# Kernel tuning notes

Measured on AMD Instinct MI355X. Metric: run time of the kernel, lower is better.

Reference implementation:

```python
import jax, jax.numpy as jnp
import numpy as np

B, D, L, H = 512, 512, 32, 300  # batch, input_dim, latent_dim, hidden_dim


def setup_inputs() -> dict:
    key = jax.random.key(0)
    ks = jax.random.split(key, 16)
    s = lambda k, *sh: jax.random.normal(k, sh, dtype=jnp.float32) * 0.05
    return {
        "x": jax.random.normal(ks[0], (B, D), dtype=jnp.float32),
        "eps": jax.random.normal(ks[1], (B, L), dtype=jnp.float32),
        "W": jax.random.normal(ks[2], (D, L), dtype=jnp.float32),  # mask (get_generator_mask -> W)
        "qz_w1": s(ks[3], D, H), "qz_b1": s(ks[4], H),
        "qz_w2": s(ks[5], H, H), "qz_b2": s(ks[6], H),
        "zm_w": s(ks[7], H, L), "zm_b": s(ks[8], L),
        "zl_w": s(ks[9], H, L), "zl_b": s(ks[10], L),
        "gen_w1": s(ks[11], L, H),               # no bias (bias=False)
        "gen_w2": s(ks[12], H, H), "gen_b2": s(ks[13], H),
        "col_w": s(ks[14], D, H), "col_b": s(ks[15], D),  # stacked column_means Linears
    }


def reference(x, eps, W, qz_w1, qz_b1, qz_w2, qz_b2, zm_w, zm_b, zl_w, zl_b,
              gen_w1, gen_w2, gen_b2, col_w, col_b):
    # encode
    h = jax.nn.relu(x @ qz_w1 + qz_b1)
    h = jax.nn.relu(h @ qz_w2 + qz_b2)
    z_mean = h @ zm_w + zm_b
    z_log_var = h @ zl_w + zl_b
    # reparameterize (eps supplied as input)
    z = z_mean + eps * jnp.exp(0.5 * z_log_var)
    # decode: per-column masked generator MLP, batched over columns j
    masked = W[:, None, :] * z[None, :, :]                 # [D, B, L]
    g = jax.nn.relu(jnp.einsum('jbl,lh->jbh', masked, gen_w1))
    g = jax.nn.relu(jnp.einsum('jbh,hk->jbk', g, gen_w2) + gen_b2)
    x_rec = jnp.einsum('jbh,jh->jb', g, col_w) + col_b[:, None]  # [D, B]
    x_mean = x_rec.T                                       # [B, D]
    return (x_mean, z, z_mean, z_log_var)
```

## Files before the change

kernel.cpp:

```cpp
#include <hip/hip_runtime.h>

#define B_ 512
#define D_ 512
#define L_ 32
#define H_ 300
#define NT 19
#define NS 10
#define G1S 308

typedef unsigned short ushort_t;
typedef __bf16 bf16x8 __attribute__((ext_vector_type(8)));
typedef float f32x4 __attribute__((ext_vector_type(4)));

union B8 { ushort_t u[8]; uint4 q; bf16x8 v; uint2 d[2]; __bf16 b[8]; };

__device__ __forceinline__ void split8(const float* fv, B8& hi, B8& lo) {
    #pragma unroll
    for (int i = 0; i < 8; ++i) {
        __bf16 h = (__bf16)fv[i];
        hi.b[i] = h;
        lo.b[i] = (__bf16)(fv[i] - (float)h);
    }
}

__global__ __launch_bounds__(64) void prep_kernel(
        const float* __restrict__ gw1, const float* __restrict__ gw2,
        const float* __restrict__ qw1, const float* __restrict__ qw2,
        const float* __restrict__ zmw, const float* __restrict__ zlw,
        ushort_t* __restrict__ gw1f, ushort_t* __restrict__ gw2f,
        ushort_t* __restrict__ w1hi, ushort_t* __restrict__ w1lo,
        ushort_t* __restrict__ w2hi, ushort_t* __restrict__ w2lo,
        ushort_t* __restrict__ w3hi, ushort_t* __restrict__ w3lo) {
    int blk = blockIdx.x;
    int l = threadIdx.x, grp = l >> 4, li = l & 15;
    if (blk < 209) {
        const float* src; int K, nt, s; ushort_t* dst;
        if (blk < 19) { nt = blk; s = 0; src = gw1; K = 32; dst = gw1f + (nt * 64 + l) * 8; }
        else { int i = blk - 19; nt = i / 10; s = i % 10; src = gw2; K = 300;
               dst = gw2f + ((nt * 10 + s) * 64 + l) * 8; }
        int n = nt * 16 + li;
        B8 V;
        #pragma unroll
        for (int i = 0; i < 8; ++i) {
            int k = 32 * s + 8 * grp + i;
            V.b[i] = (__bf16)((k < K && n < H_) ? src[k * H_ + n] : 0.f);
        }
        *reinterpret_cast<uint4*>(dst) = V.q;
    } else {
        const float* src = nullptr; int K, N, nt, s, stacked = 0;
        ushort_t *dh, *dl;
        if (blk < 513)      { int i = blk - 209; nt = i / 16; s = i % 16; src = qw1; K = 512; N = 300;
                              dh = w1hi + ((nt * 16 + s) * 64 + l) * 8; dl = w1lo + ((nt * 16 + s) * 64 + l) * 8; }
        else if (blk < 703) { int i = blk - 513; nt = i / 10; s = i % 10; src = qw2; K = 300; N = 300;
                              dh = w2hi + ((nt * 10 + s) * 64 + l) * 8; dl = w2lo + ((nt * 10 + s) * 64 + l) * 8; }
        else                { int i = blk - 703; nt = i / 10; s = i % 10; K = 300; N = 64; stacked = 1;
                              dh = w3hi + ((nt * 10 + s) * 64 + l) * 8; dl = w3lo + ((nt * 10 + s) * 64 + l) * 8; }
        int n = nt * 16 + li;
        float fv[8];
        #pragma unroll
        for (int i = 0; i < 8; ++i) {
            int k = 32 * s + 8 * grp + i;
            float v = 0.f;
            if (k < K && n < N) {
                if (!stacked) v = src[k * N + n];
                else          v = (n < 32) ? zmw[k * 32 + n] : zlw[k * 32 + (n - 32)];
            }
            fv[i] = v;
        }
        B8 Vh, Vl;
        split8(fv, Vh, Vl);
        *reinterpret_cast<uint4*>(dh) = Vh.q;
        *reinterpret_cast<uint4*>(dl) = Vl.q;
    }
}

template<int KSTEPS, bool RELU>
__global__ __launch_bounds__(256) void enc_gemm_f32(const float* __restrict__ A, int lda,
        const ushort_t* __restrict__ Whi, const ushort_t* __restrict__ Wlo,
        const float* __restrict__ bias, float* __restrict__ out, int ldo,
        int Ncols, int ntiles) {
    const int tid = threadIdx.x;
    const int w = tid >> 6, lane = tid & 63;
    const int grp = lane >> 4, li = lane & 15;
    const int r0 = blockIdx.x * 16;
    const int nt = blockIdx.y * 4 + w;
    const bool active = nt < ntiles;

    f32x4 acc = {0.f, 0.f, 0.f, 0.f};
    for (int s = 0; s < KSTEPS; ++s) {
        int kb = 32 * s + 8 * grp;
        B8 Ah, Al;
        if (kb + 8 <= lda) {
            const float* ap = A + (size_t)(r0 + li) * lda + kb;
            float4 f0 = *reinterpret_cast<const float4*>(ap);
            float4 f1 = *reinterpret_cast<const float4*>(ap + 4);
            float fv[8] = {f0.x, f0.y, f0.z, f0.w, f1.x, f1.y, f1.z, f1.w};
            split8(fv, Ah, Al);
        } else {
            Ah.q = make_uint4(0, 0, 0, 0);
            Al.q = make_uint4(0, 0, 0, 0);
        }
        if (active) {
            bf16x8 bh = *reinterpret_cast<const bf16x8*>(
                Whi + ((size_t)(nt * KSTEPS + s) * 64 + lane) * 8);
            bf16x8 bl = *reinterpret_cast<const bf16x8*>(
                Wlo + ((size_t)(nt * KSTEPS + s) * 64 + lane) * 8);
            acc = __builtin_amdgcn_mfma_f32_16x16x32_bf16(Ah.v, bh, acc, 0, 0, 0);
            acc = __builtin_amdgcn_mfma_f32_16x16x32_bf16(Al.v, bh, acc, 0, 0, 0);
            acc = __builtin_amdgcn_mfma_f32_16x16x32_bf16(Ah.v, bl, acc, 0, 0, 0);
        }
    }
    if (active) {
        int h = nt * 16 + li;
        float bv = (bias != nullptr && h < Ncols) ? bias[h] : 0.f;
        #pragma unroll
        for (int r = 0; r < 4; ++r) {
            float v = acc[r] + bv;
            if (RELU) v = fmaxf(v, 0.f);
            if (h >= Ncols) v = 0.f;
            out[(size_t)(r0 + 4 * grp + r) * ldo + h] = v;
        }
    }
}

__global__ __launch_bounds__(256) void enc3_reparam(const float* __restrict__ h2,
        const ushort_t* __restrict__ w3hi, const ushort_t* __restrict__ w3lo,
        const float* __restrict__ zmb, const float* __restrict__ zlb,
        const float* __restrict__ eps, float* __restrict__ out, float* __restrict__ zb) {
    __shared__ float zs[16][64];
    const int tid = threadIdx.x;
    const int w = tid >> 6, lane = tid & 63;
    const int grp = lane >> 4, li = lane & 15;
    const int r0 = blockIdx.x * 16;

    f32x4 acc = {0.f, 0.f, 0.f, 0.f};
    for (int s = 0; s < 10; ++s) {
        int kb = 32 * s + 8 * grp;
        B8 Ah, Al;
        if (kb + 8 <= 304) {
            const float* ap = h2 + (size_t)(r0 + li) * 304 + kb;
            float4 f0 = *reinterpret_cast<const float4*>(ap);
            float4 f1 = *reinterpret_cast<const float4*>(ap + 4);
            float fv[8] = {f0.x, f0.y, f0.z, f0.w, f1.x, f1.y, f1.z, f1.w};
            split8(fv, Ah, Al);
        } else {
            Ah.q = make_uint4(0, 0, 0, 0);
            Al.q = make_uint4(0, 0, 0, 0);
        }
        bf16x8 bh = *reinterpret_cast<const bf16x8*>(w3hi + ((size_t)(w * 10 + s) * 64 + lane) * 8);
        bf16x8 bl = *reinterpret_cast<const bf16x8*>(w3lo + ((size_t)(w * 10 + s) * 64 + lane) * 8);
        acc = __builtin_amdgcn_mfma_f32_16x16x32_bf16(Ah.v, bh, acc, 0, 0, 0);
        acc = __builtin_amdgcn_mfma_f32_16x16x32_bf16(Al.v, bh, acc, 0, 0, 0);
        acc = __builtin_amdgcn_mfma_f32_16x16x32_bf16(Ah.v, bl, acc, 0, 0, 0);
    }
    #pragma unroll
    for (int r = 0; r < 4; ++r) zs[4 * grp + r][w * 16 + li] = acc[r];
    __syncthreads();

    for (int idx = tid; idx < 512; idx += 256) {
        int m = idx >> 5, l2 = idx & 31;
        int row = r0 + m;
        float zm = zs[m][l2] + zmb[l2];
        float zl = zs[m][32 + l2] + zlb[l2];
        float zv = zm + eps[row * 32 + l2] * expf(0.5f * zl);
        out[B_ * D_ + row * 32 + l2] = zv;
        out[B_ * D_ + B_ * L_ + row * 32 + l2] = zm;
        out[B_ * D_ + 2 * B_ * L_ + row * 32 + l2] = zl;
        zb[row * 32 + l2] = zv;
    }
}

__global__ __launch_bounds__(256, 3) void decode_kernel(
        const float* __restrict__ z, const float* __restrict__ Wmask,
        const ushort_t* __restrict__ gw1f, const ushort_t* __restrict__ gw2f,
        const float* __restrict__ gb2, const float* __restrict__ colw,
        const float* __restrict__ colb, float* __restrict__ xmean) {
    __shared__ __align__(16) ushort_t g1s[64 * G1S + 16];
    __shared__ float xpart[4][64];

    const int j    = blockIdx.y;
    const int b0   = blockIdx.x * 64;
    const int tid  = threadIdx.x;
    const int w    = tid >> 6;
    const int lane = tid & 63;
    const int grp  = lane >> 4, li = lane & 15;
    const int nlocal = (w == 3) ? 4 : 5;

    B8 bm[4];
    {
        const float* wp = Wmask + (size_t)j * L_ + 8 * grp;
        float4 w0 = *reinterpret_cast<const float4*>(wp);
        float4 w1 = *reinterpret_cast<const float4*>(wp + 4);
        float wv[8] = {w0.x, w0.y, w0.z, w0.w, w1.x, w1.y, w1.z, w1.w};
        #pragma unroll
        for (int mt = 0; mt < 4; ++mt) {
            const float* zp = z + (size_t)(b0 + mt * 16 + li) * L_ + 8 * grp;
            float4 z0 = *reinterpret_cast<const float4*>(zp);
            float4 z1 = *reinterpret_cast<const float4*>(zp + 4);
            float zv[8] = {z0.x, z0.y, z0.z, z0.w, z1.x, z1.y, z1.z, z1.w};
            #pragma unroll
            for (int i = 0; i < 8; ++i) bm[mt].b[i] = (__bf16)(wv[i] * zv[i]);
        }
        for (int idx = tid; idx < 272; idx += 256) {
            if (idx < 256) g1s[(idx >> 2) * G1S + 304 + (idx & 3)] = 0;
            else           g1s[64 * G1S + (idx - 256)] = 0;
        }
    }
    __syncthreads();

    #pragma unroll
    for (int ntl = 0; ntl < 5; ++ntl) {
        if (ntl < nlocal) {
            int nt = w * 5 + ntl;
            bf16x8 ga = *reinterpret_cast<const bf16x8*>(gw1f + (nt * 64 + lane) * 8);
            #pragma unroll
            for (int mt = 0; mt < 4; ++mt) {
                f32x4 c = {0.f, 0.f, 0.f, 0.f};
                c = __builtin_amdgcn_mfma_f32_16x16x32_bf16(ga, bm[mt].v, c, 0, 0, 0);
                B8 P;
                #pragma unroll
                for (int r = 0; r < 4; ++r) P.b[r] = (__bf16)fmaxf(c[r], 0.f);
                *reinterpret_cast<uint2*>(&g1s[(mt * 16 + li) * G1S + nt * 16 + 4 * grp]) = P.d[0];
            }
        }
    }
    __syncthreads();

    {
        f32x4 acc[4][5];
        #pragma unroll
        for (int mt = 0; mt < 4; ++mt)
            #pragma unroll
            for (int n = 0; n < 5; ++n) acc[mt][n] = {0.f, 0.f, 0.f, 0.f};

        const size_t lane8 = (size_t)lane * 8;
        for (int s = 0; s < NS; ++s) {
            B8 af[4];
            #pragma unroll
            for (int mt = 0; mt < 4; ++mt) {
                const ushort_t* p = &g1s[(mt * 16 + li) * G1S + 32 * s + 8 * grp];
                af[mt].d[0] = *reinterpret_cast<const uint2*>(p);
                af[mt].d[1] = *reinterpret_cast<const uint2*>(p + 4);
            }
            #pragma unroll
            for (int ntl = 0; ntl < 5; ++ntl) {
                if (ntl < nlocal) {
                    bf16x8 bfr = *reinterpret_cast<const bf16x8*>(
                        gw2f + (size_t)((w * 5 + ntl) * NS + s) * 512 + lane8);
                    #pragma unroll
                    for (int mt = 0; mt < 4; ++mt)
                        acc[mt][ntl] = __builtin_amdgcn_mfma_f32_16x16x32_bf16(
                            af[mt].v, bfr, acc[mt][ntl], 0, 0, 0);
                }
            }
        }

        float partial[4][4] = {};
        #pragma unroll
        for (int ntl = 0; ntl < 5; ++ntl) {
            if (ntl < nlocal) {
                int h = (w * 5 + ntl) * 16 + li;
                float bias = 0.f, fac = 0.f;
                if (h < H_) { bias = gb2[h]; fac = colw[j * H_ + h]; }
                #pragma unroll
                for (int mt = 0; mt < 4; ++mt)
                    #pragma unroll
                    for (int r = 0; r < 4; ++r)
                        partial[mt][r] += fmaxf(acc[mt][ntl][r] + bias, 0.f) * fac;
            }
        }
        #pragma unroll
        for (int mt = 0; mt < 4; ++mt)
            #pragma unroll
            for (int r = 0; r < 4; ++r) {
                float v = partial[mt][r];
                v += __shfl_xor(v, 1);
                v += __shfl_xor(v, 2);
                v += __shfl_xor(v, 4);
                v += __shfl_xor(v, 8);
                if (li == 0) xpart[w][mt * 16 + 4 * grp + r] = v;
            }
    }
    __syncthreads();

    if (tid < 64) {
        float v = colb[j];
        #pragma unroll
        for (int ww = 0; ww < 4; ++ww) v += xpart[ww][tid];
        xmean[(size_t)(b0 + tid) * D_ + j] = v;
    }
}

extern "C" void kernel_launch(void* const* d_in, const int* in_sizes, int n_in,
                              void* d_out, int out_size, void* d_ws, size_t ws_size,
                              hipStream_t stream) {
    const float* x     = (const float*)d_in[0];
    const float* eps   = (const float*)d_in[1];
    const float* Wm    = (const float*)d_in[2];
    const float* qz_w1 = (const float*)d_in[3];
    const float* qz_b1 = (const float*)d_in[4];
    const float* qz_w2 = (const float*)d_in[5];
    const float* qz_b2 = (const float*)d_in[6];
    const float* zm_w  = (const float*)d_in[7];
    const float* zm_b  = (const float*)d_in[8];
    const float* zl_w  = (const float*)d_in[9];
    const float* zl_b  = (const float*)d_in[10];
    const float* gw1   = (const float*)d_in[11];
    const float* gw2   = (const float*)d_in[12];
    const float* gb2   = (const float*)d_in[13];
    const float* colw  = (const float*)d_in[14];
    const float* colb  = (const float*)d_in[15];
    float* out = (float*)d_out;
    char* ws = (char*)d_ws;

    ushort_t* gw1f = (ushort_t*)(ws + 0);
    ushort_t* gw2f = (ushort_t*)(ws + 19456);
    ushort_t* w1hi = (ushort_t*)(ws + 214016);
    ushort_t* w1lo = (ushort_t*)(ws + 525312);
    ushort_t* w2hi = (ushort_t*)(ws + 836608);
    ushort_t* w2lo = (ushort_t*)(ws + 1031168);
    ushort_t* w3hi = (ushort_t*)(ws + 1225728);
    ushort_t* w3lo = (ushort_t*)(ws + 1266688);
    float*    h1   = (float*)(ws + 1307648);
    float*    h2   = (float*)(ws + 214016);
    float*    zb   = (float*)(ws + 1930240);

    prep_kernel<<<743, 64, 0, stream>>>(gw1, gw2, qz_w1, qz_w2, zm_w, zl_w,
                                        gw1f, gw2f, w1hi, w1lo, w2hi, w2lo, w3hi, w3lo);
    enc_gemm_f32<16, true><<<dim3(32, 5), 256, 0, stream>>>(
        x, 512, w1hi, w1lo, qz_b1, h1, 304, 300, NT);
    enc_gemm_f32<10, true><<<dim3(32, 5), 256, 0, stream>>>(
        h1, 304, w2hi, w2lo, qz_b2, h2, 304, 300, NT);
    enc3_reparam<<<32, 256, 0, stream>>>(h2, w3hi, w3lo, zm_b, zl_b, eps, out, zb);
    decode_kernel<<<dim3(8, 512), 256, 0, stream>>>(zb, Wm, gw1f, gw2f, gb2, colw, colb, out);
}
```

Before: 111.9 us.

## Fuse three encoder GEMMs and reparameterization into one kernel with LDS intermediates

```diff
diff --git a/kernel.cpp b/kernel.cpp
--- a/kernel.cpp
+++ b/kernel.cpp
@@ -7,6 +7,7 @@
 #define NT 19
 #define NS 10
 #define G1S 308
+#define HS 312
 
 typedef unsigned short ushort_t;
 typedef __bf16 bf16x8 __attribute__((ext_vector_type(8)));
@@ -74,94 +75,146 @@
     }
 }
 
-template<int KSTEPS, bool RELU>
-__global__ __launch_bounds__(256) void enc_gemm_f32(const float* __restrict__ A, int lda,
-        const ushort_t* __restrict__ Whi, const ushort_t* __restrict__ Wlo,
-        const float* __restrict__ bias, float* __restrict__ out, int ldo,
-        int Ncols, int ntiles) {
+__global__ __launch_bounds__(256) void fused_encoder(
+        const float* __restrict__ x,
+        const ushort_t* __restrict__ w1hi, const ushort_t* __restrict__ w1lo,
+        const ushort_t* __restrict__ w2hi, const ushort_t* __restrict__ w2lo,
+        const ushort_t* __restrict__ w3hi, const ushort_t* __restrict__ w3lo,
+        const float* __restrict__ b1, const float* __restrict__ b2,
+        const float* __restrict__ zmb, const float* __restrict__ zlb,
+        const float* __restrict__ eps, float* __restrict__ out,
+        float* __restrict__ zb) {
+    __shared__ __align__(16) ushort_t hs1_hi[16 * HS + 16], hs1_lo[16 * HS + 16];
+    __shared__ __align__(16) ushort_t hs2_hi[16 * HS + 16], hs2_lo[16 * HS + 16];
+    __shared__ float zs2[64][17];
+
     const int tid = threadIdx.x;
     const int w = tid >> 6, lane = tid & 63;
     const int grp = lane >> 4, li = lane & 15;
     const int r0 = blockIdx.x * 16;
-    const int nt = blockIdx.y * 4 + w;
-    const bool active = nt < ntiles;
-
-    f32x4 acc = {0.f, 0.f, 0.f, 0.f};
-    for (int s = 0; s < KSTEPS; ++s) {
-        int kb = 32 * s + 8 * grp;
-        B8 Ah, Al;
-        if (kb + 8 <= lda) {
-            const float* ap = A + (size_t)(r0 + li) * lda + kb;
+    const int nlocal = (w == 3) ? 4 : 5;
+
+    for (int idx = tid; idx < 16 * 8 + 16; idx += 256) {
+        int off = (idx < 128) ? ((idx >> 3) * HS + 304 + (idx & 7)) : (16 * HS + (idx - 128));
+        hs1_hi[off] = 0; hs1_lo[off] = 0; hs2_hi[off] = 0; hs2_lo[off] = 0;
+    }
+    __syncthreads();
+
+    {
+        f32x4 acc[5];
+        #pragma unroll
+        for (int i = 0; i < 5; ++i) acc[i] = {0.f, 0.f, 0.f, 0.f};
+        for (int s = 0; s < 16; ++s) {
+            const float* ap = x + (size_t)(r0 + li) * 512 + 32 * s + 8 * grp;
             float4 f0 = *reinterpret_cast<const float4*>(ap);
             float4 f1 = *reinterpret_cast<const float4*>(ap + 4);
             float fv[8] = {f0.x, f0.y, f0.z, f0.w, f1.x, f1.y, f1.z, f1.w};
-            split8(fv, Ah, Al);
-        } else {
-            Ah.q = make_uint4(0, 0, 0, 0);
-            Al.q = make_uint4(0, 0, 0, 0);
-        }
-        if (active) {
-            bf16x8 bh = *reinterpret_cast<const bf16x8*>(
-                Whi + ((size_t)(nt * KSTEPS + s) * 64 + lane) * 8);
-            bf16x8 bl = *reinterpret_cast<const bf16x8*>(
-                Wlo + ((size_t)(nt * KSTEPS + s) * 64 + lane) * 8);
-            acc = __builtin_amdgcn_mfma_f32_16x16x32_bf16(Ah.v, bh, acc, 0, 0, 0);
-            acc = __builtin_amdgcn_mfma_f32_16x16x32_bf16(Al.v, bh, acc, 0, 0, 0);
-            acc = __builtin_amdgcn_mfma_f32_16x16x32_bf16(Ah.v, bl, acc, 0, 0, 0);
-        }
-    }
-    if (active) {
-        int h = nt * 16 + li;
-        float bv = (bias != nullptr && h < Ncols) ? bias[h] : 0.f;
-        #pragma unroll
-        for (int r = 0; r < 4; ++r) {
-            float v = acc[r] + bv;
-            if (RELU) v = fmaxf(v, 0.f);
-            if (h >= Ncols) v = 0.f;
-            out[(size_t)(r0 + 4 * grp + r) * ldo + h] = v;
-        }
-    }
-}
-
-__global__ __launch_bounds__(256) void enc3_reparam(const float* __restrict__ h2,
-        const ushort_t* __restrict__ w3hi, const ushort_t* __restrict__ w3lo,
-        const float* __restrict__ zmb, const float* __restrict__ zlb,
-        const float* __restrict__ eps, float* __restrict__ out, float* __restrict__ zb) {
-    __shared__ float zs[16][64];
-    const int tid = threadIdx.x;
-    const int w = tid >> 6, lane = tid & 63;
-    const int grp = lane >> 4, li = lane & 15;
-    const int r0 = blockIdx.x * 16;
-
-    f32x4 acc = {0.f, 0.f, 0.f, 0.f};
-    for (int s = 0; s < 10; ++s) {
-        int kb = 32 * s + 8 * grp;
-        B8 Ah, Al;
-        if (kb + 8 <= 304) {
-            const float* ap = h2 + (size_t)(r0 + li) * 304 + kb;
-            float4 f0 = *reinterpret_cast<const float4*>(ap);
-            float4 f1 = *reinterpret_cast<const float4*>(ap + 4);
-            float fv[8] = {f0.x, f0.y, f0.z, f0.w, f1.x, f1.y, f1.z, f1.w};
-            split8(fv, Ah, Al);
-        } else {
-            Ah.q = make_uint4(0, 0, 0, 0);
-            Al.q = make_uint4(0, 0, 0, 0);
-        }
-        bf16x8 bh = *reinterpret_cast<const bf16x8*>(w3hi + ((size_t)(w * 10 + s) * 64 + lane) * 8);
-        bf16x8 bl = *reinterpret_cast<const bf16x8*>(w3lo + ((size_t)(w * 10 + s) * 64 + lane) * 8);
-        acc = __builtin_amdgcn_mfma_f32_16x16x32_bf16(Ah.v, bh, acc, 0, 0, 0);
-        acc = __builtin_amdgcn_mfma_f32_16x16x32_bf16(Al.v, bh, acc, 0, 0, 0);
-        acc = __builtin_amdgcn_mfma_f32_16x16x32_bf16(Ah.v, bl, acc, 0, 0, 0);
-    }
-    #pragma unroll
-    for (int r = 0; r < 4; ++r) zs[4 * grp + r][w * 16 + li] = acc[r];
+            B8 Bh, Bl;
+            split8(fv, Bh, Bl);
+            #pragma unroll
+            for (int ntl = 0; ntl < 5; ++ntl) {
+                if (ntl < nlocal) {
+                    int nt = w * 5 + ntl;
+                    bf16x8 Ah = *reinterpret_cast<const bf16x8*>(
+                        w1hi + ((size_t)(nt * 16 + s) * 64 + lane) * 8);
+                    bf16x8 Al = *reinterpret_cast<const bf16x8*>(
+                        w1lo + ((size_t)(nt * 16 + s) * 64 + lane) * 8);
+                    acc[ntl] = __builtin_amdgcn_mfma_f32_16x16x32_bf16(Ah, Bh.v, acc[ntl], 0, 0, 0);
+                    acc[ntl] = __builtin_amdgcn_mfma_f32_16x16x32_bf16(Al, Bh.v, acc[ntl], 0, 0, 0);
+                    acc[ntl] = __builtin_amdgcn_mfma_f32_16x16x32_bf16(Ah, Bl.v, acc[ntl], 0, 0, 0);
+                }
+            }
+        }
+        #pragma unroll
+        for (int ntl = 0; ntl < 5; ++ntl) {
+            if (ntl < nlocal) {
+                int nt = w * 5 + ntl;
+                B8 Ph, Pl;
+                #pragma unroll
+                for (int r = 0; r < 4; ++r) {
+                    int h = nt * 16 + 4 * grp + r;
+                    float v = (h < H_) ? fmaxf(acc[ntl][r] + b1[h], 0.f) : 0.f;
+                    __bf16 hb = (__bf16)v;
+                    Ph.b[r] = hb;
+                    Pl.b[r] = (__bf16)(v - (float)hb);
+                }
+                int off = li * HS + nt * 16 + 4 * grp;
+                *reinterpret_cast<uint2*>(&hs1_hi[off]) = Ph.d[0];
+                *reinterpret_cast<uint2*>(&hs1_lo[off]) = Pl.d[0];
+            }
+        }
+    }
+    __syncthreads();
+
+    {
+        f32x4 acc[5];
+        #pragma unroll
+        for (int i = 0; i < 5; ++i) acc[i] = {0.f, 0.f, 0.f, 0.f};
+        for (int s = 0; s < NS; ++s) {
+            int off = li * HS + 32 * s + 8 * grp;
+            B8 Bh, Bl;
+            Bh.q = *reinterpret_cast<const uint4*>(&hs1_hi[off]);
+            Bl.q = *reinterpret_cast<const uint4*>(&hs1_lo[off]);
+            #pragma unroll
+            for (int ntl = 0; ntl < 5; ++ntl) {
+                if (ntl < nlocal) {
+                    int nt = w * 5 + ntl;
+                    bf16x8 Ah = *reinterpret_cast<const bf16x8*>(
+                        w2hi + ((size_t)(nt * 10 + s) * 64 + lane) * 8);
+                    bf16x8 Al = *reinterpret_cast<const bf16x8*>(
+                        w2lo + ((size_t)(nt * 10 + s) * 64 + lane) * 8);
+                    acc[ntl] = __builtin_amdgcn_mfma_f32_16x16x32_bf16(Ah, Bh.v, acc[ntl], 0, 0, 0);
+                    acc[ntl] = __builtin_amdgcn_mfma_f32_16x16x32_bf16(Al, Bh.v, acc[ntl], 0, 0, 0);
+                    acc[ntl] = __builtin_amdgcn_mfma_f32_16x16x32_bf16(Ah, Bl.v, acc[ntl], 0, 0, 0);
+                }
+            }
+        }
+        #pragma unroll
+        for (int ntl = 0; ntl < 5; ++ntl) {
+            if (ntl < nlocal) {
+                int nt = w * 5 + ntl;
+                B8 Ph, Pl;
+                #pragma unroll
+                for (int r = 0; r < 4; ++r) {
+                    int h = nt * 16 + 4 * grp + r;
+                    float v = (h < H_) ? fmaxf(acc[ntl][r] + b2[h], 0.f) : 0.f;
+                    __bf16 hb = (__bf16)v;
+                    Ph.b[r] = hb;
+                    Pl.b[r] = (__bf16)(v - (float)hb);
+                }
+                int off = li * HS + nt * 16 + 4 * grp;
+                *reinterpret_cast<uint2*>(&hs2_hi[off]) = Ph.d[0];
+                *reinterpret_cast<uint2*>(&hs2_lo[off]) = Pl.d[0];
+            }
+        }
+    }
+    __syncthreads();
+
+    {
+        f32x4 acc = {0.f, 0.f, 0.f, 0.f};
+        for (int s = 0; s < NS; ++s) {
+            int off = li * HS + 32 * s + 8 * grp;
+            B8 Bh, Bl;
+            Bh.q = *reinterpret_cast<const uint4*>(&hs2_hi[off]);
+            Bl.q = *reinterpret_cast<const uint4*>(&hs2_lo[off]);
+            bf16x8 Ah = *reinterpret_cast<const bf16x8*>(
+                w3hi + ((size_t)(w * 10 + s) * 64 + lane) * 8);
+            bf16x8 Al = *reinterpret_cast<const bf16x8*>(
+                w3lo + ((size_t)(w * 10 + s) * 64 + lane) * 8);
+            acc = __builtin_amdgcn_mfma_f32_16x16x32_bf16(Ah, Bh.v, acc, 0, 0, 0);
+            acc = __builtin_amdgcn_mfma_f32_16x16x32_bf16(Al, Bh.v, acc, 0, 0, 0);
+            acc = __builtin_amdgcn_mfma_f32_16x16x32_bf16(Ah, Bl.v, acc, 0, 0, 0);
+        }
+        #pragma unroll
+        for (int r = 0; r < 4; ++r) zs2[w * 16 + 4 * grp + r][li] = acc[r];
+    }
     __syncthreads();
 
     for (int idx = tid; idx < 512; idx += 256) {
         int m = idx >> 5, l2 = idx & 31;
         int row = r0 + m;
-        float zm = zs[m][l2] + zmb[l2];
-        float zl = zs[m][32 + l2] + zlb[l2];
+        float zm = zs2[l2][m] + zmb[l2];
+        float zl = zs2[32 + l2][m] + zlb[l2];
         float zv = zm + eps[row * 32 + l2] * expf(0.5f * zl);
         out[B_ * D_ + row * 32 + l2] = zv;
         out[B_ * D_ + B_ * L_ + row * 32 + l2] = zm;
@@ -208,24 +261,28 @@
     }
     __syncthreads();
 
-    #pragma unroll
-    for (int ntl = 0; ntl < 5; ++ntl) {
-        if (ntl < nlocal) {
-            int nt = w * 5 + ntl;
-            bf16x8 ga = *reinterpret_cast<const bf16x8*>(gw1f + (nt * 64 + lane) * 8);
-            #pragma unroll
-            for (int mt = 0; mt < 4; ++mt) {
-                f32x4 c = {0.f, 0.f, 0.f, 0.f};
-                c = __builtin_amdgcn_mfma_f32_16x16x32_bf16(ga, bm[mt].v, c, 0, 0, 0);
-                B8 P;
+    {
+        ushort_t* st = &g1s[li * G1S + 4 * grp];
+        #pragma unroll
+        for (int ntl = 0; ntl < 5; ++ntl) {
+            if (ntl < nlocal) {
+                int nt = w * 5 + ntl;
+                bf16x8 ga = *reinterpret_cast<const bf16x8*>(gw1f + (nt * 64 + lane) * 8);
                 #pragma unroll
-                for (int r = 0; r < 4; ++r) P.b[r] = (__bf16)fmaxf(c[r], 0.f);
-                *reinterpret_cast<uint2*>(&g1s[(mt * 16 + li) * G1S + nt * 16 + 4 * grp]) = P.d[0];
-            }
-        }
-    }
-    __syncthreads();
-
+                for (int mt = 0; mt < 4; ++mt) {
+                    f32x4 c = {0.f, 0.f, 0.f, 0.f};
+                    c = __builtin_amdgcn_mfma_f32_16x16x32_bf16(ga, bm[mt].v, c, 0, 0, 0);
+                    B8 P;
+                    #pragma unroll
+                    for (int r = 0; r < 4; ++r) P.b[r] = (__bf16)fmaxf(c[r], 0.f);
+                    *reinterpret_cast<uint2*>(st + mt * 16 * G1S + nt * 16) = P.d[0];
+                }
+            }
+        }
+    }
+    __syncthreads();
+
+    float partial[4][4] = {};
     {
         f32x4 acc[4][5];
         #pragma unroll
@@ -255,7 +312,6 @@
             }
         }
 
-        float partial[4][4] = {};
         #pragma unroll
         for (int ntl = 0; ntl < 5; ++ntl) {
             if (ntl < nlocal) {
@@ -269,18 +325,18 @@
                         partial[mt][r] += fmaxf(acc[mt][ntl][r] + bias, 0.f) * fac;
             }
         }
-        #pragma unroll
-        for (int mt = 0; mt < 4; ++mt)
-            #pragma unroll
-            for (int r = 0; r < 4; ++r) {
-                float v = partial[mt][r];
-                v += __shfl_xor(v, 1);
-                v += __shfl_xor(v, 2);
-                v += __shfl_xor(v, 4);
-                v += __shfl_xor(v, 8);
-                if (li == 0) xpart[w][mt * 16 + 4 * grp + r] = v;
-            }
-    }
+    }
+    #pragma unroll
+    for (int mt = 0; mt < 4; ++mt)
+        #pragma unroll
+        for (int r = 0; r < 4; ++r) {
+            float v = partial[mt][r];
+            v += __shfl_xor(v, 1);
+            v += __shfl_xor(v, 2);
+            v += __shfl_xor(v, 4);
+            v += __shfl_xor(v, 8);
+            if (li == 0) xpart[w][mt * 16 + 4 * grp + r] = v;
+        }
     __syncthreads();
 
     if (tid < 64) {
@@ -321,16 +377,11 @@
     ushort_t* w2lo = (ushort_t*)(ws + 1031168);
     ushort_t* w3hi = (ushort_t*)(ws + 1225728);
     ushort_t* w3lo = (ushort_t*)(ws + 1266688);
-    float*    h1   = (float*)(ws + 1307648);
-    float*    h2   = (float*)(ws + 214016);
-    float*    zb   = (float*)(ws + 1930240);
+    float*    zb   = (float*)(ws + 1307648);
 
     prep_kernel<<<743, 64, 0, stream>>>(gw1, gw2, qz_w1, qz_w2, zm_w, zl_w,
                                         gw1f, gw2f, w1hi, w1lo, w2hi, w2lo, w3hi, w3lo);
-    enc_gemm_f32<16, true><<<dim3(32, 5), 256, 0, stream>>>(
-        x, 512, w1hi, w1lo, qz_b1, h1, 304, 300, NT);
-    enc_gemm_f32<10, true><<<dim3(32, 5), 256, 0, stream>>>(
-        h1, 304, w2hi, w2lo, qz_b2, h2, 304, 300, NT);
-    enc3_reparam<<<32, 256, 0, stream>>>(h2, w3hi, w3lo, zm_b, zl_b, eps, out, zb);
+    fused_encoder<<<32, 256, 0, stream>>>(x, w1hi, w1lo, w2hi, w2lo, w3hi, w3lo,
+                                          qz_b1, qz_b2, zm_b, zl_b, eps, out, zb);
     decode_kernel<<<dim3(8, 512), 256, 0, stream>>>(zb, Wm, gw1f, gw2f, gb2, colw, colb, out);
 }
```

After: 115.5 us. 1.03x slower.

## Give each wave its own 16 batch rows in decode, removing block barriers

Applied to the files above, without the earlier changes.

```diff
diff --git a/kernel.cpp b/kernel.cpp
--- a/kernel.cpp
+++ b/kernel.cpp
@@ -6,7 +6,7 @@
 #define H_ 300
 #define NT 19
 #define NS 10
-#define G1S 308
+#define G1S 312
 
 typedef unsigned short ushort_t;
 typedef __bf16 bf16x8 __attribute__((ext_vector_type(8)));
@@ -175,8 +175,7 @@
         const ushort_t* __restrict__ gw1f, const ushort_t* __restrict__ gw2f,
         const float* __restrict__ gb2, const float* __restrict__ colw,
         const float* __restrict__ colb, float* __restrict__ xmean) {
-    __shared__ __align__(16) ushort_t g1s[64 * G1S + 16];
-    __shared__ float xpart[4][64];
+    __shared__ __align__(16) ushort_t g1s[64 * G1S];
 
     const int j    = blockIdx.y;
     const int b0   = blockIdx.x * 64;
@@ -184,110 +183,85 @@
     const int w    = tid >> 6;
     const int lane = tid & 63;
     const int grp  = lane >> 4, li = lane & 15;
-    const int nlocal = (w == 3) ? 4 : 5;
-
-    B8 bm[4];
+    const int rb   = w * 16;
+
+    B8 bm;
     {
         const float* wp = Wmask + (size_t)j * L_ + 8 * grp;
         float4 w0 = *reinterpret_cast<const float4*>(wp);
         float4 w1 = *reinterpret_cast<const float4*>(wp + 4);
         float wv[8] = {w0.x, w0.y, w0.z, w0.w, w1.x, w1.y, w1.z, w1.w};
-        #pragma unroll
-        for (int mt = 0; mt < 4; ++mt) {
-            const float* zp = z + (size_t)(b0 + mt * 16 + li) * L_ + 8 * grp;
-            float4 z0 = *reinterpret_cast<const float4*>(zp);
-            float4 z1 = *reinterpret_cast<const float4*>(zp + 4);
-            float zv[8] = {z0.x, z0.y, z0.z, z0.w, z1.x, z1.y, z1.z, z1.w};
+        const float* zp = z + (size_t)(b0 + rb + li) * L_ + 8 * grp;
+        float4 z0 = *reinterpret_cast<const float4*>(zp);
+        float4 z1 = *reinterpret_cast<const float4*>(zp + 4);
+        float zv[8] = {z0.x, z0.y, z0.z, z0.w, z1.x, z1.y, z1.z, z1.w};
+        #pragma unroll
+        for (int i = 0; i < 8; ++i) bm.b[i] = (__bf16)(wv[i] * zv[i]);
+        int zr = rb + (lane >> 2), zc = 304 + (lane & 3);
+        g1s[zr * G1S + zc]     = 0;
+        g1s[zr * G1S + zc + 4] = 0;
+    }
+
+    #pragma unroll
+    for (int nt = 0; nt < NT; ++nt) {
+        bf16x8 ga = *reinterpret_cast<const bf16x8*>(gw1f + (nt * 64 + lane) * 8);
+        f32x4 c = {0.f, 0.f, 0.f, 0.f};
+        c = __builtin_amdgcn_mfma_f32_16x16x32_bf16(ga, bm.v, c, 0, 0, 0);
+        B8 P;
+        #pragma unroll
+        for (int r = 0; r < 4; ++r) P.b[r] = (__bf16)fmaxf(c[r], 0.f);
+        *reinterpret_cast<uint2*>(&g1s[(rb + li) * G1S + nt * 16 + 4 * grp]) = P.d[0];
+    }
+
+    float partial[4] = {0.f, 0.f, 0.f, 0.f};
+    const size_t lane8 = (size_t)lane * 8;
+    #pragma unroll
+    for (int p = 0; p < 2; ++p) {
+        const int nbase = p * 10;
+        const int npass = p ? 9 : 10;
+        f32x4 acc[10];
+        #pragma unroll
+        for (int i = 0; i < 10; ++i) acc[i] = {0.f, 0.f, 0.f, 0.f};
+
+        for (int s = 0; s < NS; ++s) {
+            int kb = 32 * s + 8 * grp;
+            if (kb > 304) kb = 304;
+            const ushort_t* pA = &g1s[(rb + li) * G1S + kb];
+            B8 af;
+            af.d[0] = *reinterpret_cast<const uint2*>(pA);
+            af.d[1] = *reinterpret_cast<const uint2*>(pA + 4);
             #pragma unroll
-            for (int i = 0; i < 8; ++i) bm[mt].b[i] = (__bf16)(wv[i] * zv[i]);
-        }
-        for (int idx = tid; idx < 272; idx += 256) {
-            if (idx < 256) g1s[(idx >> 2) * G1S + 304 + (idx & 3)] = 0;
-            else           g1s[64 * G1S + (idx - 256)] = 0;
-        }
-    }
-    __syncthreads();
-
-    #pragma unroll
-    for (int ntl = 0; ntl < 5; ++ntl) {
-        if (ntl < nlocal) {
-            int nt = w * 5 + ntl;
-            bf16x8 ga = *reinterpret_cast<const bf16x8*>(gw1f + (nt * 64 + lane) * 8);
-            #pragma unroll
-            for (int mt = 0; mt < 4; ++mt) {
-                f32x4 c = {0.f, 0.f, 0.f, 0.f};
-                c = __builtin_amdgcn_mfma_f32_16x16x32_bf16(ga, bm[mt].v, c, 0, 0, 0);
-                B8 P;
-                #pragma unroll
-                for (int r = 0; r < 4; ++r) P.b[r] = (__bf16)fmaxf(c[r], 0.f);
-                *reinterpret_cast<uint2*>(&g1s[(mt * 16 + li) * G1S + nt * 16 + 4 * grp]) = P.d[0];
-            }
-        }
-    }
-    __syncthreads();
-
-    {
-        f32x4 acc[4][5];
-        #pragma unroll
-        for (int mt = 0; mt < 4; ++mt)
-            #pragma unroll
-            for (int n = 0; n < 5; ++n) acc[mt][n] = {0.f, 0.f, 0.f, 0.f};
-
-        const size_t lane8 = (size_t)lane * 8;
-        for (int s = 0; s < NS; ++s) {
-            B8 af[4];
-            #pragma unroll
-            for (int mt = 0; mt < 4; ++mt) {
-                const ushort_t* p = &g1s[(mt * 16 + li) * G1S + 32 * s + 8 * grp];
-                af[mt].d[0] = *reinterpret_cast<const uint2*>(p);
-                af[mt].d[1] = *reinterpret_cast<const uint2*>(p + 4);
-            }
-            #pragma unroll
-            for (int ntl = 0; ntl < 5; ++ntl) {
-                if (ntl < nlocal) {
+            for (int ntl = 0; ntl < 10; ++ntl) {
+                if (ntl < npass) {
                     bf16x8 bfr = *reinterpret_cast<const bf16x8*>(
-                        gw2f + (size_t)((w * 5 + ntl) * NS + s) * 512 + lane8);
-                    #pragma unroll
-                    for (int mt = 0; mt < 4; ++mt)
-                        acc[mt][ntl] = __builtin_amdgcn_mfma_f32_16x16x32_bf16(
-                            af[mt].v, bfr, acc[mt][ntl], 0, 0, 0);
+                        gw2f + (size_t)((nbase + ntl) * NS + s) * 512 + lane8);
+                    acc[ntl] = __builtin_amdgcn_mfma_f32_16x16x32_bf16(
+                        af.v, bfr, acc[ntl], 0, 0, 0);
                 }
             }
         }
-
-        float partial[4][4] = {};
-        #pragma unroll
-        for (int ntl = 0; ntl < 5; ++ntl) {
-            if (ntl < nlocal) {
-                int h = (w * 5 + ntl) * 16 + li;
+        #pragma unroll
+        for (int ntl = 0; ntl < 10; ++ntl) {
+            if (ntl < npass) {
+                int h = (nbase + ntl) * 16 + li;
                 float bias = 0.f, fac = 0.f;
                 if (h < H_) { bias = gb2[h]; fac = colw[j * H_ + h]; }
                 #pragma unroll
-                for (int mt = 0; mt < 4; ++mt)
-                    #pragma unroll
-                    for (int r = 0; r < 4; ++r)
-                        partial[mt][r] += fmaxf(acc[mt][ntl][r] + bias, 0.f) * fac;
+                for (int r = 0; r < 4; ++r)
+                    partial[r] += fmaxf(acc[ntl][r] + bias, 0.f) * fac;
             }
         }
-        #pragma unroll
-        for (int mt = 0; mt < 4; ++mt)
-            #pragma unroll
-            for (int r = 0; r < 4; ++r) {
-                float v = partial[mt][r];
-                v += __shfl_xor(v, 1);
-                v += __shfl_xor(v, 2);
-                v += __shfl_xor(v, 4);
-                v += __shfl_xor(v, 8);
-                if (li == 0) xpart[w][mt * 16 + 4 * grp + r] = v;
-            }
-    }
-    __syncthreads();
-
-    if (tid < 64) {
-        float v = colb[j];
-        #pragma unroll
-        for (int ww = 0; ww < 4; ++ww) v += xpart[ww][tid];
-        xmean[(size_t)(b0 + tid) * D_ + j] = v;
+    }
+
+    #pragma unroll
+    for (int r = 0; r < 4; ++r) {
+        float v = partial[r];
+        v += __shfl_xor(v, 1);
+        v += __shfl_xor(v, 2);
+        v += __shfl_xor(v, 4);
+        v += __shfl_xor(v, 8);
+        if (li == 0)
+            xmean[(size_t)(b0 + rb + 4 * grp + r) * D_ + j] = v + colb[j];
     }
 }
 
```

New measurement: 208.4 us. 1.86x slower.
